# Kernel optimization log

Measured on AMD Instinct MI355X. Metric: run time of the kernel, lower is better.

## Reference

```python
import jax, jax.numpy as jnp
import numpy as np

B, S, D, H, O = 8, 4096, 512, 512, 512
NS, NC, SD = 4, 4, 8
CLIP, TEMP, SUP_SCALE, SUP_EPS, LN_EPS = 3.0, 1.0, 1.0, 1e-4, 1e-5


def _ln(x, w, b):
    m = jnp.mean(x, -1, keepdims=True)
    v = jnp.mean((x - m) ** 2, -1, keepdims=True)
    return (x - m) * jax.lax.rsqrt(v + LN_EPS) * w + b


def _lin(x, w, b):
    return x @ w.T + b


def setup_inputs() -> dict:
    key = jax.random.key(0)
    ks = iter(jax.random.split(key, 32))

    def W(shape):
        return 0.02 * jax.random.normal(next(ks), shape, jnp.float32)

    inp = {}
    inp['x'] = jax.random.normal(next(ks), (B, S, D), jnp.float32)
    inp['sb_norm_w'] = jnp.ones((D,), jnp.float32)
    inp['sb_norm_b'] = jnp.zeros((D,), jnp.float32)
    inp['sb_proj_w'] = W((NS, D)); inp['sb_proj_b'] = jnp.zeros((NS,), jnp.float32)
    inp['sb_sum_w'] = W((SD, 4)); inp['sb_sum_b'] = jnp.zeros((SD,), jnp.float32)
    inp['cb_norm_w'] = jnp.ones((D,), jnp.float32)
    inp['cb_norm_b'] = jnp.zeros((D,), jnp.float32)
    inp['cb_proj_w'] = W((NC, D)); inp['cb_proj_b'] = jnp.zeros((NC,), jnp.float32)
    inp['cb_sum_w'] = W((SD, 4)); inp['cb_sum_b'] = jnp.zeros((SD,), jnp.float32)
    inp['vn_norm_w'] = jnp.ones((D,), jnp.float32)
    inp['vn_norm_b'] = jnp.zeros((D,), jnp.float32)
    inp['vn_w1'] = W((H, D)); inp['vn_b1'] = jnp.zeros((H,), jnp.float32)
    inp['vn_w2'] = W((O, H)); inp['vn_b2'] = jnp.zeros((O,), jnp.float32)
    inp['un_norm_w'] = jnp.ones((D,), jnp.float32)
    inp['un_norm_b'] = jnp.zeros((D,), jnp.float32)
    inp['un_w1'] = W((H, D)); inp['un_b1'] = jnp.zeros((H,), jnp.float32)
    inp['un_w2'] = W((1, H)); inp['un_b2'] = jnp.zeros((1,), jnp.float32)
    inp['en_w'] = W((H, 1)); inp['en_b'] = jnp.zeros((H,), jnp.float32)
    inp['pr_w'] = W((H, 1)); inp['pr_b'] = jnp.zeros((H,), jnp.float32)
    inp['rs_w'] = W((H, 1)); inp['rs_b'] = jnp.zeros((H,), jnp.float32)
    inp['ssp_w'] = W((H, SD)); inp['ssp_b'] = jnp.zeros((H,), jnp.float32)
    inp['csp_w'] = W((H, SD)); inp['csp_b'] = jnp.zeros((H,), jnp.float32)
    inp['out_w'] = W((O, O + 5 * H)); inp['out_b'] = jnp.zeros((O,), jnp.float32)
    inp['support_logits'] = jnp.zeros((NS,), jnp.float32)
    inp['conflict_weights'] = jnp.ones((NC,), jnp.float32)
    inp['drive_bias'] = jnp.zeros((1,), jnp.float32)
    inp['bias_resistance'] = jnp.zeros((1,), jnp.float32)
    inp['update_threshold'] = jnp.ones((1,), jnp.float32)
    inp['eml_gamma'] = jnp.full((1,), 0.3, jnp.float32)
    inp['eml_lambda'] = jnp.ones((1,), jnp.float32)
    inp['eml_bias'] = jnp.zeros((1,), jnp.float32)
    return inp


def reference(x, sb_norm_w, sb_norm_b, sb_proj_w, sb_proj_b, sb_sum_w, sb_sum_b,
              cb_norm_w, cb_norm_b, cb_proj_w, cb_proj_b, cb_sum_w, cb_sum_b,
              vn_norm_w, vn_norm_b, vn_w1, vn_b1, vn_w2, vn_b2,
              un_norm_w, un_norm_b, un_w1, un_b1, un_w2, un_b2,
              en_w, en_b, pr_w, pr_b, rs_w, rs_b,
              ssp_w, ssp_b, csp_w, csp_b, out_w, out_b,
              support_logits, conflict_weights, drive_bias, bias_resistance,
              update_threshold, eml_gamma, eml_lambda, eml_bias):
    # Support bank: LN -> Linear -> softplus(+eps) -> stats -> summary Linear
    sf = jax.nn.softplus(_lin(_ln(x, sb_norm_w, sb_norm_b), sb_proj_w, sb_proj_b)) + SUP_EPS  # [B,S,NS]
    ls = jnp.log(sf)
    s_seed = jnp.concatenate([
        sf.mean(-1, keepdims=True), sf.std(-1, keepdims=True),
        ls.mean(-1, keepdims=True), ls.max(-1, keepdims=True)], -1)
    ss = _lin(s_seed, sb_sum_w, sb_sum_b)  # [B,S,SD]
    # Conflict bank
    cf = jax.nn.softplus(_lin(_ln(x, cb_norm_w, cb_norm_b), cb_proj_w, cb_proj_b))  # [B,S,NC]
    c_seed = jnp.concatenate([
        cf.mean(-1, keepdims=True), cf.std(-1, keepdims=True),
        cf.max(-1, keepdims=True), cf.min(-1, keepdims=True)], -1)
    cs = _lin(c_seed, cb_sum_w, cb_sum_b)  # [B,S,SD]
    # Drive / resistance
    sw = jax.nn.softmax(support_logits)
    drive = drive_bias + SUP_SCALE * (ls * sw).sum(-1, keepdims=True) / np.sqrt(NS)
    cw = jax.nn.softplus(conflict_weights)
    weighted_conflict = (cf * cw).sum(-1, keepdims=True) / np.sqrt(NC)
    u_h = jax.nn.gelu(_lin(_ln(x, un_norm_w, un_norm_b), un_w1, un_b1), approximate=False)
    uncertainty = jax.nn.softplus(_lin(u_h, un_w2, un_b2))  # [B,S,1]
    resistance = bias_resistance + weighted_conflict + uncertainty
    # EML unit (dim=1): bounded linear drive-resistance balance, warmup_eta=1.0
    e_raw = eml_gamma * drive - eml_lambda * resistance + eml_bias
    energy = CLIP * jnp.tanh(e_raw / CLIP)
    activation = jax.nn.sigmoid(energy / TEMP)
    precision = jax.nn.softplus(energy - update_threshold)
    # Value net
    v_h = jax.nn.gelu(_lin(_ln(x, vn_norm_w, vn_norm_b), vn_w1, vn_b1), approximate=False)
    value = _lin(v_h, vn_w2, vn_b2)  # [B,S,O]
    feats = jnp.concatenate([
        activation * value,
        _lin(energy, en_w, en_b),
        _lin(precision, pr_w, pr_b),
        _lin(resistance, rs_w, rs_b),
        _lin(ss, ssp_w, ssp_b),
        _lin(cs, csp_w, csp_b)], -1)  # [B,S,O+5H]
    return _lin(feats, out_w, out_b)  # [B,S,O]
```

## Files before the change

### kernel.cpp

```cpp
#include <hip/hip_runtime.h>
#include <stdint.h>

typedef unsigned short u16;
typedef __bf16 bf16x8 __attribute__((ext_vector_type(8)));
typedef float f32x4 __attribute__((ext_vector_type(4)));
typedef __attribute__((address_space(1))) void gvoid;
typedef __attribute__((address_space(3))) void lvoid;

#define NTOK 32768

#define FENCE() asm volatile("" ::: "memory")
#define SBAR()  do { FENCE(); __builtin_amdgcn_s_barrier(); FENCE(); } while (0)
#define SVM4()  asm volatile("s_waitcnt vmcnt(4)" ::: "memory")
#define SVM0()  asm volatile("s_waitcnt vmcnt(0)" ::: "memory")

__device__ __forceinline__ u16 f2bf(float f) {
    unsigned u = __float_as_uint(f);
    u += 0x7fffu + ((u >> 16) & 1u);
    return (u16)(u >> 16);
}
__device__ __forceinline__ float softplusf(float x) {
    return fmaxf(x, 0.f) + log1pf(expf(-fabsf(x)));
}
__device__ __forceinline__ float geluf(float x) {
    return 0.5f * x * (1.f + erff(x * 0.7071067811865475f));
}
__device__ __forceinline__ float wave_sum(float v) {
#pragma unroll
    for (int o = 32; o > 0; o >>= 1) v += __shfl_xor(v, o);
    return v;
}
__device__ __forceinline__ float blk_sum(float v) {
    __shared__ float sm[4];
    v = wave_sum(v);
    __syncthreads();
    if ((threadIdx.x & 63) == 0) sm[threadIdx.x >> 6] = v;
    __syncthreads();
    return sm[0] + sm[1] + sm[2] + sm[3];
}

__global__ void k_prep(
    const float* __restrict__ x, u16* __restrict__ Ybf,
    const float* __restrict__ vnw1, const float* __restrict__ vnnw, const float* __restrict__ vnnb, const float* __restrict__ vnb1,
    const float* __restrict__ unw1, const float* __restrict__ unnw, const float* __restrict__ unnb, const float* __restrict__ unb1,
    const float* __restrict__ sbpw, const float* __restrict__ sbpb, const float* __restrict__ sbnw, const float* __restrict__ sbnb,
    const float* __restrict__ cbpw, const float* __restrict__ cbpb, const float* __restrict__ cbnw, const float* __restrict__ cbnb,
    const float* __restrict__ outw, const float* __restrict__ enw, const float* __restrict__ enb,
    const float* __restrict__ prw, const float* __restrict__ prb,
    const float* __restrict__ rsw, const float* __restrict__ rsb,
    const float* __restrict__ sspw, const float* __restrict__ sspb,
    const float* __restrict__ cspw, const float* __restrict__ cspb,
    const float* __restrict__ vnw2, const float* __restrict__ vnb2,
    u16* __restrict__ Astk, float* __restrict__ bstk, float* __restrict__ pb,
    u16* __restrict__ Aow, u16* __restrict__ vnT,
    float* __restrict__ a_en, float* __restrict__ a_pr, float* __restrict__ a_rs,
    float* __restrict__ b_vo, float* __restrict__ c_cn, float* __restrict__ Mss, float* __restrict__ Mcs)
{
    const int t = threadIdx.x;
    if (blockIdx.x < NTOK / 4) {
        const int w = t >> 6, l = t & 63;
        const int n = blockIdx.x * 4 + w;
        const float* xr = x + (size_t)n * 512;
        float4 xa = *(const float4*)(xr + 4 * l);
        float4 xb = *(const float4*)(xr + 256 + 4 * l);
        float v[8] = {xa.x, xa.y, xa.z, xa.w, xb.x, xb.y, xb.z, xb.w};
        float s1 = 0.f, s2 = 0.f;
#pragma unroll
        for (int c = 0; c < 8; c++) { s1 += v[c]; s2 += v[c] * v[c]; }
        s1 = wave_sum(s1); s2 = wave_sum(s2);
        const float mean = s1 * (1.f / 512.f);
        const float var = s2 * (1.f / 512.f) - mean * mean;
        const float rstd = rsqrtf(var + 1e-5f);
        float y[8];
#pragma unroll
        for (int c = 0; c < 8; c++) y[c] = (v[c] - mean) * rstd;
        *(ushort4*)(Ybf + (size_t)n * 512 + 4 * l) = make_ushort4(f2bf(y[0]), f2bf(y[1]), f2bf(y[2]), f2bf(y[3]));
        *(ushort4*)(Ybf + (size_t)n * 512 + 256 + 4 * l) = make_ushort4(f2bf(y[4]), f2bf(y[5]), f2bf(y[6]), f2bf(y[7]));
        return;
    }
    const int b = blockIdx.x - NTOK / 4;
    if (b < 1024) {
        const float *w1, *nw, *nb; float bias;
        if (b < 512) { w1 = vnw1 + (size_t)b * 512; nw = vnnw; nb = vnnb; bias = vnb1[b]; }
        else { int r = b - 512; w1 = unw1 + (size_t)r * 512; nw = unnw; nb = unnb; bias = unb1[r]; }
        float part = 0.f;
        for (int d = t; d < 512; d += 256) {
            float wv = w1[d];
            Astk[(size_t)b * 512 + d] = f2bf(wv * nw[d]);
            part += wv * nb[d];
        }
        float s = blk_sum(part);
        if (t == 0) bstk[b] = bias + s;
    } else if (b < 1032) {
        int j = b - 1024;
        const float *pw, *nw, *nb; float bias;
        if (j < 4) { pw = sbpw + j * 512; nw = sbnw; nb = sbnb; bias = sbpb[j]; }
        else { pw = cbpw + (j - 4) * 512; nw = cbnw; nb = cbnb; bias = cbpb[j - 4]; }
        float part = 0.f;
        for (int d = t; d < 512; d += 256) {
            float wv = pw[d];
            Astk[(size_t)(1024 + j) * 512 + d] = f2bf(wv * nw[d]);
            part += wv * nb[d];
        }
        float s = blk_sum(part);
        if (t == 0) pb[j] = bias + s;
    } else if (b < 1152) {
        for (int d = t; d < 512; d += 256) Astk[(size_t)b * 512 + d] = 0;
    } else if (b < 1664) {
        int i = b - 1152;
        const float* ow = outw + (size_t)i * 3072;
        float pen = 0, ppr = 0, prs = 0, pbv = 0, pcc = 0;
        float pms[8], pmc[8];
#pragma unroll
        for (int k = 0; k < 8; k++) { pms[k] = 0.f; pmc[k] = 0.f; }
        for (int h = t; h < 512; h += 256) {
            float o0 = ow[h];        Aow[(size_t)i * 512 + h] = f2bf(o0); pbv += o0 * vnb2[h];
            float o1 = ow[512 + h];  pen += o1 * enw[h]; pcc += o1 * enb[h];
            float o2 = ow[1024 + h]; ppr += o2 * prw[h]; pcc += o2 * prb[h];
            float o3 = ow[1536 + h]; prs += o3 * rsw[h]; pcc += o3 * rsb[h];
            float o4 = ow[2048 + h]; pcc += o4 * sspb[h];
            float o5 = ow[2560 + h]; pcc += o5 * cspb[h];
#pragma unroll
            for (int k = 0; k < 8; k++) { pms[k] += o4 * sspw[h * 8 + k]; pmc[k] += o5 * cspw[h * 8 + k]; }
        }
        float r;
        r = blk_sum(pen); if (t == 0) a_en[i] = r;
        r = blk_sum(ppr); if (t == 0) a_pr[i] = r;
        r = blk_sum(prs); if (t == 0) a_rs[i] = r;
        r = blk_sum(pbv); if (t == 0) b_vo[i] = r;
        r = blk_sum(pcc); if (t == 0) c_cn[i] = r;
        for (int k = 0; k < 8; k++) { r = blk_sum(pms[k]); if (t == 0) Mss[i * 8 + k] = r; }
        for (int k = 0; k < 8; k++) { r = blk_sum(pmc[k]); if (t == 0) Mcs[i * 8 + k] = r; }
    } else {
        int hrow = b - 1664;
        for (int o = t; o < 512; o += 256)
            vnT[(size_t)hrow * 512 + o] = f2bf(vnw2[(size_t)o * 512 + hrow]);
    }
}

__device__ __forceinline__ void load_bfrag8(const u16* bufB, bf16x8 (&bfrag)[4][2], int wn, int l) {
#pragma unroll
    for (int nt = 0; nt < 4; nt++) {
        const int row = wn * 64 + nt * 16 + (l & 15);
#pragma unroll
        for (int ks = 0; ks < 2; ks++) {
            const int s = (ks * 4 + (l >> 4)) ^ (row & 7);
            bfrag[nt][ks] = *(const bf16x8*)(bufB + row * 64 + (s << 3));
        }
    }
}

template <int Q>
__device__ __forceinline__ void load_aquad8(const u16* bufA, bf16x8 (&af)[2], int wm, int l) {
    const int row = wm * 64 + Q * 16 + (l & 15);
#pragma unroll
    for (int ks = 0; ks < 2; ks++) {
        const int s = (ks * 4 + (l >> 4)) ^ (row & 7);
        af[ks] = *(const bf16x8*)(bufA + row * 64 + (s << 3));
    }
}

template <int Q>
__device__ __forceinline__ void do_mfma8(bf16x8 (&af)[2], bf16x8 (&bfrag)[4][2], f32x4 (&acc)[4][4]) {
#pragma unroll
    for (int nt = 0; nt < 4; nt++)
#pragma unroll
        for (int ks = 0; ks < 2; ks++)
            acc[Q][nt] = __builtin_amdgcn_mfma_f32_16x16x32_bf16(af[ks], bfrag[nt][ks], acc[Q][nt], 0, 0, 0);
}

#define PHASE8(Q, bufA_, bufB_, READB, STAGE_STMT, VM_STMT)       \
    do {                                                          \
        if (READB) load_bfrag8(bufB_, bfrag, wn, l);              \
        bf16x8 af[2];                                             \
        load_aquad8<Q>(bufA_, af, wm, l);                         \
        STAGE_STMT;                                               \
        SBAR();                                                   \
        __builtin_amdgcn_s_setprio(1);                            \
        do_mfma8<Q>(af, bfrag, acc);                              \
        __builtin_amdgcn_s_setprio(0);                            \
        VM_STMT;                                                  \
        SBAR();                                                   \
    } while (0)

__device__ __forceinline__ void gemm8_mainloop(const u16* __restrict__ Ag, const u16* __restrict__ Bg,
                                               size_t arow0, size_t brow0,
                                               u16* sm, f32x4 (&acc)[4][4], int w, int l)
{
    const int wm = w >> 1, wn = w & 1;
    u16* const sA0 = sm;
    u16* const sA1 = sm + 8192;
    u16* const sB0 = sm + 16384;
    u16* const sB1 = sm + 24576;
    const int rchunk = l >> 3;
    const int gc = (((l & 7) ^ ((l >> 3) & 7)) << 3);

    auto STG = [&](const u16* g, size_t rb, int tile, u16* lbase) {
        const int kt = tile * 64;
#pragma unroll
        for (int i = 0; i < 4; i++) {
            const int r0 = (w * 4 + i) * 8;
            __builtin_amdgcn_global_load_lds(
                (gvoid*)const_cast<u16*>(g + (rb + r0 + rchunk) * 512 + kt + gc),
                (lvoid*)(lbase + r0 * 64), 16, 0, 0);
        }
    };

    STG(Ag, arow0, 0, sA0);
    STG(Bg, brow0, 0, sB0);
    STG(Bg, brow0, 1, sB1);
    SVM4();
    SBAR();

    bf16x8 bfrag[4][2];
    for (int it = 0; it < 4; ++it) {
        const int t1 = 2 * it + 1, t2 = 2 * it + 2, t3 = 2 * it + 3;
        const bool lastit = (it == 3);
        PHASE8(0, sA0, sB0, true,  { STG(Ag, arow0, t1, sA1); }, );
        PHASE8(1, sA0, sB0, false, { if (t2 < 8) STG(Bg, brow0, t2, sB0); }, );
        PHASE8(2, sA0, sB0, false, { }, );
        PHASE8(3, sA0, sB0, false, { }, { if (lastit) { SVM0(); } else { SVM4(); } });
        PHASE8(0, sA1, sB1, true,  { if (t2 < 8) STG(Ag, arow0, t2, sA0); }, );
        PHASE8(1, sA1, sB1, false, { if (t3 < 8) STG(Bg, brow0, t3, sB1); }, );
        PHASE8(2, sA1, sB1, false, { }, );
        PHASE8(3, sA1, sB1, false, { }, { SVM4(); });
    }
}

__global__ __launch_bounds__(256, 2) void k_gemm1(const u16* __restrict__ Y, const u16* __restrict__ Ast,
                                                  const float* __restrict__ bstk, const float* __restrict__ pb,
                                                  const float* __restrict__ unw2,
                                                  const u16* __restrict__ Aow, const u16* __restrict__ vnT,
                                                  u16* __restrict__ Wvo,
                                                  u16* __restrict__ H, float* __restrict__ wp,
                                                  float* __restrict__ wdotp)
{
    __shared__ __align__(16) u16 smem[32768];
    const f32x4 zero = {0.f, 0.f, 0.f, 0.f};
    f32x4 acc[4][4];
#pragma unroll
    for (int a = 0; a < 4; a++)
#pragma unroll
        for (int c = 0; c < 4; c++) acc[a][c] = zero;
    const int nwg = gridDim.x * gridDim.y;
    const int lin = blockIdx.y * gridDim.x + blockIdx.x;
    const int swz = (lin & 7) * (nwg >> 3) + (lin >> 3);
    const int by = swz / gridDim.x, bx = swz % gridDim.x;
    const int t = threadIdx.x, w = t >> 6, l = t & 63;
    const int wr = ((w >> 1) << 6), wc = ((w & 1) << 6);
    const int lr = ((l >> 4) << 2), lc = l & 15;

    if (bx == 9) {
        if (by >= 16) return;
        gemm8_mainloop(Aow, vnT, (size_t)(by >> 2) * 128, (size_t)(by & 3) * 128, smem, acc, w, l);
        const int rbase = (by >> 2) * 128 + wr;
        const int cbase = (by & 3) * 128 + wc;
#pragma unroll
        for (int rt = 0; rt < 4; rt++)
#pragma unroll
            for (int ct = 0; ct < 4; ct++)
#pragma unroll
                for (int j = 0; j < 4; j++)
                    Wvo[(size_t)(rbase + rt * 16 + lr + j) * 512 + cbase + ct * 16 + lc] = f2bf(acc[rt][ct][j]);
        return;
    }

    gemm8_mainloop(Y, Ast, (size_t)by * 128, (size_t)bx * 128, smem, acc, w, l);

    if (bx == 8) {
        if ((w & 1) == 0 && lc < 8) {
            const float bv = pb[lc];
            const int rbase = by * 128 + wr;
#pragma unroll
            for (int rt = 0; rt < 4; rt++)
#pragma unroll
                for (int j = 0; j < 4; j++) {
                    const int n = rbase + rt * 16 + lr + j;
                    wp[(size_t)n * 8 + lc] = acc[rt][0][j] + bv;
                }
        }
        return;
    }
    if (bx >= 4) {
        const int cb = (bx - 4) * 128;
        float part[4][4];
#pragma unroll
        for (int rt = 0; rt < 4; rt++)
#pragma unroll
            for (int j = 0; j < 4; j++) part[rt][j] = 0.f;
#pragma unroll
        for (int ct = 0; ct < 4; ct++) {
            const int col = cb + wc + ct * 16 + lc;
            const float bv = bstk[512 + col];
            const float w2 = unw2[col];
#pragma unroll
            for (int rt = 0; rt < 4; rt++)
#pragma unroll
                for (int j = 0; j < 4; j++)
                    part[rt][j] += geluf(acc[rt][ct][j] + bv) * w2;
        }
        float* sf = (float*)smem;
        const int slot = ((w & 1) << 4) | lc;
        __syncthreads();
#pragma unroll
        for (int rt = 0; rt < 4; rt++)
#pragma unroll
            for (int j = 0; j < 4; j++)
                sf[(wr + rt * 16 + lr + j) * 32 + slot] = part[rt][j];
        __syncthreads();
        if (t < 128) {
            float s = 0.f;
#pragma unroll
            for (int k2 = 0; k2 < 32; k2++) s += sf[t * 32 + k2];
            wdotp[(size_t)(bx - 4) * NTOK + by * 128 + t] = s;
        }
        return;
    }
    __syncthreads();
#pragma unroll
    for (int ct = 0; ct < 4; ct++) {
        const int col = wc + ct * 16 + lc;
        const float bv = bstk[bx * 128 + col];
#pragma unroll
        for (int rt = 0; rt < 4; rt++) {
            const int row = wr + rt * 16 + lr;
#pragma unroll
            for (int j = 0; j < 4; j++)
                smem[(row + j) * 136 + col] = f2bf(geluf(acc[rt][ct][j] + bv));
        }
    }
    __syncthreads();
    const size_t gbase = (size_t)(by * 128) * 512 + bx * 128;
#pragma unroll
    for (int jj = 0; jj < 8; jj++) {
        const int r = jj * 16 + (t >> 4), u = t & 15;
        bf16x8 vv = *(const bf16x8*)(smem + r * 136 + u * 8);
        *(bf16x8*)(H + gbase + (size_t)r * 512 + u * 8) = vv;
    }
}

__global__ __launch_bounds__(256, 2) void k_gemm2(const u16* __restrict__ H, const u16* __restrict__ Wvo,
    const float* __restrict__ wp, const float* __restrict__ wdotp,
    const float* __restrict__ unb2,
    const float* __restrict__ sbsw, const float* __restrict__ sbsb,
    const float* __restrict__ cbsw, const float* __restrict__ cbsb,
    const float* __restrict__ suplog, const float* __restrict__ confw,
    const float* __restrict__ drvb, const float* __restrict__ biasres,
    const float* __restrict__ emlg, const float* __restrict__ emll,
    const float* __restrict__ emlb, const float* __restrict__ updthr,
    const float* __restrict__ a_en, const float* __restrict__ a_pr, const float* __restrict__ a_rs,
    const float* __restrict__ b_vo, const float* __restrict__ c_cn,
    const float* __restrict__ Mss, const float* __restrict__ Mcs,
    const float* __restrict__ outb, float* __restrict__ out)
{
    __shared__ __align__(16) u16 smem[32768];
    __shared__ float sbank[128 * 20];
    const f32x4 zero = {0.f, 0.f, 0.f, 0.f};
    f32x4 acc[4][4];
#pragma unroll
    for (int a = 0; a < 4; a++)
#pragma unroll
        for (int c = 0; c < 4; c++) acc[a][c] = zero;
    const int nwg = gridDim.x * gridDim.y;
    const int lin = blockIdx.y * gridDim.x + blockIdx.x;
    const int swz = (lin & 7) * (nwg >> 3) + (lin >> 3);
    const int by = swz / gridDim.x, bx = swz % gridDim.x;
    const int t = threadIdx.x, w = t >> 6, l = t & 63;

    if (t < 128) {
        const int n = by * 128 + t;
        float4 p0 = *(const float4*)(wp + (size_t)n * 8);
        float4 p1 = *(const float4*)(wp + (size_t)n * 8 + 4);
        float p[8] = {p0.x, p0.y, p0.z, p0.w, p1.x, p1.y, p1.z, p1.w};
        const float dot = wdotp[n] + wdotp[NTOK + n] + wdotp[2 * NTOK + n] + wdotp[3 * NTOK + n];
        float sf[4], lsv[4], cf[4];
#pragma unroll
        for (int j = 0; j < 4; j++) {
            sf[j] = softplusf(p[j]) + 1e-4f;
            lsv[j] = logf(sf[j]);
            cf[j] = softplusf(p[j + 4]);
        }
        const float smn = 0.25f * (sf[0] + sf[1] + sf[2] + sf[3]);
        float sd = 0.f;
#pragma unroll
        for (int j = 0; j < 4; j++) sd += (sf[j] - smn) * (sf[j] - smn);
        const float sstd = sqrtf(0.25f * sd);
        const float lmn = 0.25f * (lsv[0] + lsv[1] + lsv[2] + lsv[3]);
        const float lmx = fmaxf(fmaxf(lsv[0], lsv[1]), fmaxf(lsv[2], lsv[3]));
        const float cmn = 0.25f * (cf[0] + cf[1] + cf[2] + cf[3]);
        float cd = 0.f;
#pragma unroll
        for (int j = 0; j < 4; j++) cd += (cf[j] - cmn) * (cf[j] - cmn);
        const float cstd = sqrtf(0.25f * cd);
        const float cmx = fmaxf(fmaxf(cf[0], cf[1]), fmaxf(cf[2], cf[3]));
        const float cmi = fminf(fminf(cf[0], cf[1]), fminf(cf[2], cf[3]));
        float seed_s[4] = {smn, sstd, lmn, lmx};
        float seed_c[4] = {cmn, cstd, cmx, cmi};
#pragma unroll
        for (int k = 0; k < 8; k++) {
            float a = sbsb[k], b2 = cbsb[k];
#pragma unroll
            for (int j = 0; j < 4; j++) { a += sbsw[k * 4 + j] * seed_s[j]; b2 += cbsw[k * 4 + j] * seed_c[j]; }
            sbank[t * 20 + 4 + k] = a;
            sbank[t * 20 + 12 + k] = b2;
        }
        float mx = fmaxf(fmaxf(suplog[0], suplog[1]), fmaxf(suplog[2], suplog[3]));
        float e[4], se = 0.f;
#pragma unroll
        for (int j = 0; j < 4; j++) { e[j] = expf(suplog[j] - mx); se += e[j]; }
        float dv = 0.f, wcv = 0.f;
#pragma unroll
        for (int j = 0; j < 4; j++) { dv += lsv[j] * (e[j] / se); wcv += cf[j] * softplusf(confw[j]); }
        const float drive = drvb[0] + 0.5f * dv;
        const float unc = softplusf(dot + unb2[0]);
        const float res = biasres[0] + 0.5f * wcv + unc;
        const float er = emlg[0] * drive - emll[0] * res + emlb[0];
        const float energy = 3.f * tanhf(er * (1.f / 3.f));
        sbank[t * 20 + 0] = 1.f / (1.f + expf(-energy));
        sbank[t * 20 + 1] = energy;
        sbank[t * 20 + 2] = softplusf(energy - updthr[0]);
        sbank[t * 20 + 3] = res;
    }
    __syncthreads();

    gemm8_mainloop(H, Wvo, (size_t)by * 128, (size_t)bx * 128, smem, acc, w, l);

    const int rl0 = ((w >> 1) << 6);
    const int cbase = bx * 128 + ((w & 1) << 6);
    const int lr = ((l >> 4) << 2), lc = l & 15;
    float bvo4[4], aen4[4], apr4[4], ars4[4], cc4[4], ms4[4][8], mc4[4][8];
#pragma unroll
    for (int ct = 0; ct < 4; ct++) {
        const int i = cbase + ct * 16 + lc;
        bvo4[ct] = b_vo[i]; aen4[ct] = a_en[i]; apr4[ct] = a_pr[i]; ars4[ct] = a_rs[i];
        cc4[ct] = c_cn[i] + outb[i];
#pragma unroll
        for (int k = 0; k < 8; k++) { ms4[ct][k] = Mss[i * 8 + k]; mc4[ct][k] = Mcs[i * 8 + k]; }
    }
#pragma unroll
    for (int rt = 0; rt < 4; rt++)
#pragma unroll
        for (int j = 0; j < 4; j++) {
            const int nl = rl0 + rt * 16 + lr + j;
            const size_t n = (size_t)by * 128 + nl;
            const float act = sbank[nl * 20 + 0];
            const float eng = sbank[nl * 20 + 1];
            const float prc = sbank[nl * 20 + 2];
            const float res = sbank[nl * 20 + 3];
#pragma unroll
            for (int ct = 0; ct < 4; ct++) {
                const int i = cbase + ct * 16 + lc;
                float o = act * (acc[rt][ct][j] + bvo4[ct]) + eng * aen4[ct] + prc * apr4[ct]
                        + res * ars4[ct] + cc4[ct];
#pragma unroll
                for (int k = 0; k < 8; k++)
                    o += ms4[ct][k] * sbank[nl * 20 + 4 + k] + mc4[ct][k] * sbank[nl * 20 + 12 + k];
                out[n * 512 + i] = o;
            }
        }
}

extern "C" void kernel_launch(void* const* d_in, const int* in_sizes, int n_in,
                              void* d_out, int out_size, void* d_ws, size_t ws_size,
                              hipStream_t stream)
{
    const float* x       = (const float*)d_in[0];
    const float* sbnw    = (const float*)d_in[1];
    const float* sbnb    = (const float*)d_in[2];
    const float* sbpw    = (const float*)d_in[3];
    const float* sbpb    = (const float*)d_in[4];
    const float* sbsw    = (const float*)d_in[5];
    const float* sbsb    = (const float*)d_in[6];
    const float* cbnw    = (const float*)d_in[7];
    const float* cbnb    = (const float*)d_in[8];
    const float* cbpw    = (const float*)d_in[9];
    const float* cbpb    = (const float*)d_in[10];
    const float* cbsw    = (const float*)d_in[11];
    const float* cbsb    = (const float*)d_in[12];
    const float* vnnw    = (const float*)d_in[13];
    const float* vnnb    = (const float*)d_in[14];
    const float* vnw1    = (const float*)d_in[15];
    const float* vnb1    = (const float*)d_in[16];
    const float* vnw2    = (const float*)d_in[17];
    const float* vnb2    = (const float*)d_in[18];
    const float* unnw    = (const float*)d_in[19];
    const float* unnb    = (const float*)d_in[20];
    const float* unw1    = (const float*)d_in[21];
    const float* unb1    = (const float*)d_in[22];
    const float* unw2    = (const float*)d_in[23];
    const float* unb2    = (const float*)d_in[24];
    const float* enw     = (const float*)d_in[25];
    const float* enb     = (const float*)d_in[26];
    const float* prw     = (const float*)d_in[27];
    const float* prb     = (const float*)d_in[28];
    const float* rsw     = (const float*)d_in[29];
    const float* rsb     = (const float*)d_in[30];
    const float* sspw    = (const float*)d_in[31];
    const float* sspb    = (const float*)d_in[32];
    const float* cspw    = (const float*)d_in[33];
    const float* cspb    = (const float*)d_in[34];
    const float* outw    = (const float*)d_in[35];
    const float* outb    = (const float*)d_in[36];
    const float* suplog  = (const float*)d_in[37];
    const float* confw   = (const float*)d_in[38];
    const float* drvb    = (const float*)d_in[39];
    const float* biasres = (const float*)d_in[40];
    const float* updthr  = (const float*)d_in[41];
    const float* emlg    = (const float*)d_in[42];
    const float* emll    = (const float*)d_in[43];
    const float* emlb    = (const float*)d_in[44];
    float* out = (float*)d_out;
    (void)in_sizes; (void)n_in; (void)out_size; (void)ws_size;

    char* wsp = (char*)d_ws;
    size_t off = 0;
    auto alloc = [&](size_t bytes) { char* p = wsp + off; off = (off + bytes + 255) & ~(size_t)255; return p; };
    u16*  Ybf  = (u16*)alloc((size_t)NTOK * 512 * 2);
    u16*  Hbf  = (u16*)alloc((size_t)NTOK * 512 * 2);
    u16*  Astk = (u16*)alloc(1152 * 512 * 2);
    float* bstk = (float*)alloc(1024 * 4);
    float* pb   = (float*)alloc(8 * 4);
    u16*  Aow  = (u16*)alloc(512 * 512 * 2);
    u16*  vnT  = (u16*)alloc(512 * 512 * 2);
    u16*  Wvo  = (u16*)alloc(512 * 512 * 2);
    float* a_en = (float*)alloc(512 * 4);
    float* a_pr = (float*)alloc(512 * 4);
    float* a_rs = (float*)alloc(512 * 4);
    float* b_vo = (float*)alloc(512 * 4);
    float* c_cn = (float*)alloc(512 * 4);
    float* Mss  = (float*)alloc(512 * 8 * 4);
    float* Mcs  = (float*)alloc(512 * 8 * 4);
    float* wp   = (float*)alloc((size_t)NTOK * 8 * 4);
    float* wdotp= (float*)alloc((size_t)NTOK * 4 * 4);

    k_prep<<<NTOK / 4 + 2176, 256, 0, stream>>>(x, Ybf,
                                     vnw1, vnnw, vnnb, vnb1, unw1, unnw, unnb, unb1,
                                     sbpw, sbpb, sbnw, sbnb, cbpw, cbpb, cbnw, cbnb,
                                     outw, enw, enb, prw, prb, rsw, rsb, sspw, sspb, cspw, cspb,
                                     vnw2, vnb2,
                                     Astk, bstk, pb, Aow, vnT, a_en, a_pr, a_rs, b_vo, c_cn, Mss, Mcs);
    k_gemm1<<<dim3(10, 256), 256, 0, stream>>>(Ybf, Astk, bstk, pb, unw2, Aow, vnT, Wvo,
                                               Hbf, wp, wdotp);
    k_gemm2<<<dim3(4, 256), 256, 0, stream>>>(Hbf, Wvo, wp, wdotp, unb2, sbsw, sbsb, cbsw, cbsb,
                                              suplog, confw, drvb, biasres, emlg, emll, emlb, updthr,
                                              a_en, a_pr, a_rs, b_vo, c_cn, Mss, Mcs, outb, out);
}
```

Before: 153.5 us.

## Pre-swizzle stacked weights into MFMA fragment layout and load B directly to registers

The prep kernel now writes the stacked first-layer weight matrix in a fragment-ordered layout, using a shared-memory transpose per 16-row group. GEMM1 gets a new mainloop that stages only the activation tile through LDS and reads weight fragments straight from global memory into registers, double-buffered. The goal is to halve LDS traffic and LDS footprint per K-step. In exchange each block reads weight data from global/L2 without LDS reuse, carries more register pressure, and drops the 2-blocks-per-CU launch bound.

```diff
diff --git a/kernel.cpp b/kernel.cpp
--- a/kernel.cpp
+++ b/kernel.cpp
@@ -38,6 +38,7 @@
     __syncthreads();
     return sm[0] + sm[1] + sm[2] + sm[3];
 }
+
 
 __global__ void k_prep(
     const float* __restrict__ x, u16* __restrict__ Ybf,
@@ -51,11 +52,12 @@
     const float* __restrict__ sspw, const float* __restrict__ sspb,
     const float* __restrict__ cspw, const float* __restrict__ cspb,
     const float* __restrict__ vnw2, const float* __restrict__ vnb2,
-    u16* __restrict__ Astk, float* __restrict__ bstk, float* __restrict__ pb,
+    u16* __restrict__ AstkF, float* __restrict__ bstk, float* __restrict__ pb,
     u16* __restrict__ Aow, u16* __restrict__ vnT,
     float* __restrict__ a_en, float* __restrict__ a_pr, float* __restrict__ a_rs,
     float* __restrict__ b_vo, float* __restrict__ c_cn, float* __restrict__ Mss, float* __restrict__ Mcs)
 {
+    __shared__ u16 sfrag[16 * 520];
     const int t = threadIdx.x;
     if (blockIdx.x < NTOK / 4) {
         const int w = t >> 6, l = t & 63;
@@ -79,35 +81,51 @@
         return;
     }
     const int b = blockIdx.x - NTOK / 4;
-    if (b < 1024) {
-        const float *w1, *nw, *nb; float bias;
-        if (b < 512) { w1 = vnw1 + (size_t)b * 512; nw = vnnw; nb = vnnb; bias = vnb1[b]; }
-        else { int r = b - 512; w1 = unw1 + (size_t)r * 512; nw = unnw; nb = unnb; bias = unb1[r]; }
-        float part = 0.f;
-        for (int d = t; d < 512; d += 256) {
-            float wv = w1[d];
-            Astk[(size_t)b * 512 + d] = f2bf(wv * nw[d]);
-            part += wv * nb[d];
-        }
-        float s = blk_sum(part);
-        if (t == 0) bstk[b] = bias + s;
-    } else if (b < 1032) {
-        int j = b - 1024;
-        const float *pw, *nw, *nb; float bias;
-        if (j < 4) { pw = sbpw + j * 512; nw = sbnw; nb = sbnb; bias = sbpb[j]; }
-        else { pw = cbpw + (j - 4) * 512; nw = cbnw; nb = cbnb; bias = cbpb[j - 4]; }
-        float part = 0.f;
-        for (int d = t; d < 512; d += 256) {
-            float wv = pw[d];
-            Astk[(size_t)(1024 + j) * 512 + d] = f2bf(wv * nw[d]);
-            part += wv * nb[d];
-        }
-        float s = blk_sum(part);
-        if (t == 0) pb[j] = bias + s;
-    } else if (b < 1152) {
-        for (int d = t; d < 512; d += 256) Astk[(size_t)b * 512 + d] = 0;
-    } else if (b < 1664) {
-        int i = b - 1152;
+    if (b < 72) {
+        const int g = b;
+        const int w = t >> 6, l = t & 63;
+        for (int rr = 0; rr < 4; rr++) {
+            const int lrow = w * 4 + rr;
+            const int row = g * 16 + lrow;
+            const float *src = nullptr, *nw = nullptr, *nb = nullptr;
+            float bias = 0.f;
+            if (row < 512)       { src = vnw1 + (size_t)row * 512; nw = vnnw; nb = vnnb; bias = vnb1[row]; }
+            else if (row < 1024) { int r = row - 512; src = unw1 + (size_t)r * 512; nw = unnw; nb = unnb; bias = unb1[r]; }
+            else if (row < 1032) {
+                int j = row - 1024;
+                if (j < 4) { src = sbpw + j * 512; nw = sbnw; nb = sbnb; bias = sbpb[j]; }
+                else       { src = cbpw + (j - 4) * 512; nw = cbnw; nb = cbnb; bias = cbpb[j - 4]; }
+            }
+            if (src) {
+                float part = 0.f;
+#pragma unroll
+                for (int e = 0; e < 8; e++) {
+                    const int d = l * 8 + e;
+                    float wv = src[d];
+                    sfrag[lrow * 520 + d] = f2bf(wv * nw[d]);
+                    part += wv * nb[d];
+                }
+                part = wave_sum(part);
+                if (l == 0) {
+                    if (row < 1024) bstk[row] = bias + part;
+                    else pb[row - 1024] = bias + part;
+                }
+            } else {
+#pragma unroll
+                for (int e = 0; e < 8; e++) sfrag[lrow * 520 + l * 8 + e] = 0;
+            }
+        }
+        __syncthreads();
+#pragma unroll
+        for (int q = 0; q < 4; q++) {
+            const int kt = w * 4 + q;
+            bf16x8 v = *(const bf16x8*)(sfrag + (l & 15) * 520 + kt * 32 + (l >> 4) * 8);
+            *(bf16x8*)(AstkF + ((size_t)(g * 16 + kt) * 64 + l) * 8) = v;
+        }
+        return;
+    }
+    if (b < 584) {
+        int i = b - 72;
         const float* ow = outw + (size_t)i * 3072;
         float pen = 0, ppr = 0, prs = 0, pbv = 0, pcc = 0;
         float pms[8], pmc[8];
@@ -132,9 +150,71 @@
         for (int k = 0; k < 8; k++) { r = blk_sum(pms[k]); if (t == 0) Mss[i * 8 + k] = r; }
         for (int k = 0; k < 8; k++) { r = blk_sum(pmc[k]); if (t == 0) Mcs[i * 8 + k] = r; }
     } else {
-        int hrow = b - 1664;
+        int hrow = b - 584;
         for (int o = t; o < 512; o += 256)
             vnT[(size_t)hrow * 512 + o] = f2bf(vnw2[(size_t)o * 512 + hrow]);
+    }
+}
+
+__device__ __forceinline__ void stg_a128(const u16* __restrict__ Ag, size_t arow0, int tile,
+                                         u16* lbase, int w, int l)
+{
+    const int kt = tile * 64;
+    const int rchunk = l >> 3;
+    const int gc = (((l & 7) ^ ((l >> 3) & 7)) << 3);
+#pragma unroll
+    for (int i = 0; i < 4; i++) {
+        const int r0 = (w * 4 + i) * 8;
+        __builtin_amdgcn_global_load_lds(
+            (gvoid*)const_cast<u16*>(Ag + (arow0 + r0 + rchunk) * 512 + kt + gc),
+            (lvoid*)(lbase + r0 * 64), 16, 0, 0);
+    }
+}
+
+__device__ __forceinline__ void gemm_bfrag(const u16* __restrict__ Ag, size_t arow0,
+                                           const u16* __restrict__ BF, int rtb,
+                                           u16* sm, f32x4 (&acc)[4][4], int w, int l)
+{
+    const int wm = w >> 1;
+    u16* const sA0 = sm;
+    u16* const sA1 = sm + 8192;
+
+    bf16x8 bb[2][4][2];
+    auto loadB = [&](int buf, int kt) {
+#pragma unroll
+        for (int nt = 0; nt < 4; nt++)
+#pragma unroll
+            for (int ks = 0; ks < 2; ks++)
+                bb[buf][nt][ks] = *(const bf16x8*)(BF + ((size_t)((rtb + nt) * 16 + kt * 2 + ks) * 64 + l) * 8);
+    };
+
+    stg_a128(Ag, arow0, 0, sA0, w, l);
+    loadB(0, 0);
+    __syncthreads();
+#pragma unroll
+    for (int t8 = 0; t8 < 8; t8++) {
+        const int cur = t8 & 1;
+        if (t8 < 7) {
+            loadB(cur ^ 1, t8 + 1);
+            stg_a128(Ag, arow0, t8 + 1, (t8 & 1) ? sA0 : sA1, w, l);
+        }
+        const u16* bufA = (t8 & 1) ? sA1 : sA0;
+#pragma unroll
+        for (int Q = 0; Q < 4; Q++) {
+            const int row = wm * 64 + Q * 16 + (l & 15);
+            bf16x8 af[2];
+#pragma unroll
+            for (int ks = 0; ks < 2; ks++) {
+                const int s = (ks * 4 + (l >> 4)) ^ (row & 7);
+                af[ks] = *(const bf16x8*)(bufA + row * 64 + (s << 3));
+            }
+#pragma unroll
+            for (int nt = 0; nt < 4; nt++)
+#pragma unroll
+                for (int ks = 0; ks < 2; ks++)
+                    acc[Q][nt] = __builtin_amdgcn_mfma_f32_16x16x32_bf16(af[ks], bb[cur][nt][ks], acc[Q][nt], 0, 0, 0);
+        }
+        __syncthreads();
     }
 }
 
@@ -227,13 +307,13 @@
     }
 }
 
-__global__ __launch_bounds__(256, 2) void k_gemm1(const u16* __restrict__ Y, const u16* __restrict__ Ast,
-                                                  const float* __restrict__ bstk, const float* __restrict__ pb,
-                                                  const float* __restrict__ unw2,
-                                                  const u16* __restrict__ Aow, const u16* __restrict__ vnT,
-                                                  u16* __restrict__ Wvo,
-                                                  u16* __restrict__ H, float* __restrict__ wp,
-                                                  float* __restrict__ wdotp)
+__global__ __launch_bounds__(256) void k_gemm1(const u16* __restrict__ Y, const u16* __restrict__ AstkF,
+                                               const float* __restrict__ bstk, const float* __restrict__ pb,
+                                               const float* __restrict__ unw2,
+                                               const u16* __restrict__ Aow, const u16* __restrict__ vnT,
+                                               u16* __restrict__ Wvo,
+                                               u16* __restrict__ H, float* __restrict__ wp,
+                                               float* __restrict__ wdotp)
 {
     __shared__ __align__(16) u16 smem[32768];
     const f32x4 zero = {0.f, 0.f, 0.f, 0.f};
@@ -265,7 +345,7 @@
         return;
     }
 
-    gemm8_mainloop(Y, Ast, (size_t)by * 128, (size_t)bx * 128, smem, acc, w, l);
+    gemm_bfrag(Y, (size_t)by * 128, AstkF, bx * 8 + (w & 1) * 4, smem, acc, w, l);
 
     if (bx == 8) {
         if ((w & 1) == 0 && lc < 8) {
@@ -517,7 +597,7 @@
     auto alloc = [&](size_t bytes) { char* p = wsp + off; off = (off + bytes + 255) & ~(size_t)255; return p; };
     u16*  Ybf  = (u16*)alloc((size_t)NTOK * 512 * 2);
     u16*  Hbf  = (u16*)alloc((size_t)NTOK * 512 * 2);
-    u16*  Astk = (u16*)alloc(1152 * 512 * 2);
+    u16*  AstkF= (u16*)alloc(1152 * 512 * 2);
     float* bstk = (float*)alloc(1024 * 4);
     float* pb   = (float*)alloc(8 * 4);
     u16*  Aow  = (u16*)alloc(512 * 512 * 2);
@@ -533,13 +613,13 @@
     float* wp   = (float*)alloc((size_t)NTOK * 8 * 4);
     float* wdotp= (float*)alloc((size_t)NTOK * 4 * 4);
 
-    k_prep<<<NTOK / 4 + 2176, 256, 0, stream>>>(x, Ybf,
+    k_prep<<<NTOK / 4 + 1096, 256, 0, stream>>>(x, Ybf,
                                      vnw1, vnnw, vnnb, vnb1, unw1, unnw, unnb, unb1,
                                      sbpw, sbpb, sbnw, sbnb, cbpw, cbpb, cbnw, cbnb,
                                      outw, enw, enb, prw, prb, rsw, rsb, sspw, sspb, cspw, cspb,
                                      vnw2, vnb2,
-                                     Astk, bstk, pb, Aow, vnT, a_en, a_pr, a_rs, b_vo, c_cn, Mss, Mcs);
-    k_gemm1<<<dim3(10, 256), 256, 0, stream>>>(Ybf, Astk, bstk, pb, unw2, Aow, vnT, Wvo,
+                                     AstkF, bstk, pb, Aow, vnT, a_en, a_pr, a_rs, b_vo, c_cn, Mss, Mcs);
+    k_gemm1<<<dim3(10, 256), 256, 0, stream>>>(Ybf, AstkF, bstk, pb, unw2, Aow, vnT, Wvo,
                                                Hbf, wp, wdotp);
     k_gemm2<<<dim3(4, 256), 256, 0, stream>>>(Hbf, Wvo, wp, wdotp, unb2, sbsw, sbsb, cbsw, cbsb,
                                               suplog, confw, drvb, biasres, emlg, emll, emlb, updthr,
```

New measurement: 188.7 us, median of 3. 22.9% more time.
